# Kernel optimization log

Hardware: AMD Instinct MI355X
Metric: run time of the kernel (lower is better)

The kernel has to match this reference:

```python
import jax, jax.numpy as jnp
import numpy as np

BATCH = 32768
TEXT_DIM = 384
HIDDEN = 256
NUM_LAYERS = 4
NUM_VERTS = 12
K_NN = 6


def _build_template():
    """Icosphere vertices (12, normalized) and row-normalized kNN adjacency (12,12)."""
    phi = (1.0 + 5.0 ** 0.5) / 2.0
    v = np.array([
        [-1, phi, 0], [1, phi, 0], [-1, -phi, 0], [1, -phi, 0],
        [0, -1, phi], [0, 1, phi], [0, -1, -phi], [0, 1, -phi],
        [phi, 0, -1], [phi, 0, 1], [-phi, 0, -1], [-phi, 0, 1],
    ], dtype=np.float32)
    v = v / np.linalg.norm(v, axis=1, keepdims=True)
    dist = np.linalg.norm(v[:, None, :] - v[None, :, :], axis=-1)  # (12,12)
    # k+1 smallest per row; index 0 is self (distance 0), skip it
    idx = np.argsort(dist, axis=1, kind='stable')[:, 1:K_NN + 1]
    adj = np.zeros((NUM_VERTS, NUM_VERTS), dtype=np.float32)
    rows = np.repeat(np.arange(NUM_VERTS), K_NN)
    adj[rows, idx.reshape(-1)] = 1.0
    adj = adj / (adj.sum(axis=1, keepdims=True) + 1e-6)
    return jnp.asarray(v), jnp.asarray(adj)


def setup_inputs() -> dict:
    key = jax.random.key(0)
    ks = jax.random.split(key, 8)
    template, adjacency = _build_template()
    scale = 0.02
    return {
        "text_emb": jax.random.normal(ks[0], (BATCH, TEXT_DIM), dtype=jnp.float32),
        "W_text": jax.random.normal(ks[1], (TEXT_DIM, HIDDEN), dtype=jnp.float32) * scale,
        "b_text": jnp.zeros((HIDDEN,), dtype=jnp.float32),
        "W_gnn": jax.random.normal(ks[2], (NUM_LAYERS, HIDDEN, HIDDEN), dtype=jnp.float32) * scale,
        "b_gnn": jnp.zeros((NUM_LAYERS, HIDDEN), dtype=jnp.float32),
        "W_out": jax.random.normal(ks[3], (HIDDEN, 3), dtype=jnp.float32) * scale,
        "b_out": jnp.zeros((3,), dtype=jnp.float32),
        "adjacency": adjacency,   # (12,12) buffer
        "template": template,     # (12,3) buffer
    }


def reference(text_emb, W_text, b_text, W_gnn, b_gnn, W_out, b_out, adjacency, template):
    # text projection -> broadcast to all nodes
    tf = text_emb @ W_text + b_text                       # (B, H)
    B = text_emb.shape[0]
    h = jnp.broadcast_to(tf[:, None, :], (B, NUM_VERTS, HIDDEN))
    # GNN layers: aggregate (shared adjacency across batch), project, relu
    for l in range(NUM_LAYERS):
        agg = jnp.einsum('nm,bmd->bnd', adjacency, h)     # (B, 12, H)
        h = jax.nn.relu(agg @ W_gnn[l] + b_gnn[l])
    displacements = h @ W_out + b_out                     # (B, 12, 3)
    return template[None, :, :] + displacements
```

## Files before the change

### kernel.cpp

```cpp
#include <hip/hip_runtime.h>
#include <stdint.h>

#define TD      384
#define HID     256

typedef __bf16 bf16;
typedef __attribute__((ext_vector_type(8))) __bf16 bf16x8;
typedef __attribute__((ext_vector_type(4))) float f32x4;

union FragU { uint4 u; bf16x8 f; };
union PackU { uint4 u; bf16 v[8]; };

__device__ inline f32x4 mfma16(bf16x8 a, bf16x8 b, f32x4 c) {
  return __builtin_amdgcn_mfma_f32_16x16x32_bf16(a, b, c, 0, 0, 0);
}

__global__ __launch_bounds__(256) void prep_all(
    const float* __restrict__ W_text, const float* __restrict__ b_text,
    const float* __restrict__ W_gnn, const float* __restrict__ b_gnn,
    const float* __restrict__ W_out,
    bf16* __restrict__ wt_f, bf16* __restrict__ wt_g,
    float* __restrict__ wot, float* __restrict__ bfv)
{
  const int bid = blockIdx.x, tid = threadIdx.x;
  const float* g0 = W_gnn;
  if (bid < 48) {
    const int k0 = bid * 8;
    const int n = tid;
    float a0=0.f,a1=0.f,a2=0.f,a3=0.f,a4=0.f,a5=0.f,a6=0.f,a7=0.f;
    for (int j = 0; j < HID; j += 8) {
      #pragma unroll
      for (int u = 0; u < 8; u++) {
        float g = g0[(size_t)(j + u) * HID + n];
        a0 += W_text[(size_t)(k0 + 0) * HID + j + u] * g;
        a1 += W_text[(size_t)(k0 + 1) * HID + j + u] * g;
        a2 += W_text[(size_t)(k0 + 2) * HID + j + u] * g;
        a3 += W_text[(size_t)(k0 + 3) * HID + j + u] * g;
        a4 += W_text[(size_t)(k0 + 4) * HID + j + u] * g;
        a5 += W_text[(size_t)(k0 + 5) * HID + j + u] * g;
        a6 += W_text[(size_t)(k0 + 6) * HID + j + u] * g;
        a7 += W_text[(size_t)(k0 + 7) * HID + j + u] * g;
      }
    }
    PackU pk;
    pk.v[0]=(bf16)a0; pk.v[1]=(bf16)a1; pk.v[2]=(bf16)a2; pk.v[3]=(bf16)a3;
    pk.v[4]=(bf16)a4; pk.v[5]=(bf16)a5; pk.v[6]=(bf16)a6; pk.v[7]=(bf16)a7;
    int idx = ((n >> 4) * 48 + bid) * 16 + (n & 15);
    *(uint4*)(wt_f + idx * 8) = pk.u;
  } else if (bid < 144) {
    int idx = (bid - 48) * 256 + tid;
    int cc = idx & 15, c = idx >> 4;
    int l = c >> 9, c2 = c & 511;
    int oct = c2 & 31;
    int n = (c2 >> 5) * 16 + cc;
    const float* base = W_gnn + (size_t)(l + 1) * HID * HID;
    PackU pk;
    #pragma unroll
    for (int j = 0; j < 8; j++) pk.v[j] = (bf16)base[(oct * 8 + j) * HID + n];
    *(uint4*)(wt_g + idx * 8) = pk.u;
  } else {
    int n = tid;
    float s0 = 0.f, s1 = 0.f;
    for (int j = 0; j < HID; j += 2) {
      s0 += b_text[j]     * g0[(size_t)j * HID + n];
      s1 += b_text[j + 1] * g0[(size_t)(j + 1) * HID + n];
    }
    bfv[n] = s0 + s1 + b_gnn[n];
    #pragma unroll
    for (int t = tid; t < 3 * HID; t += 256) {
      int comp = t >> 8, k = t & 255;
      wot[comp * HID + k] = W_out[k * 3 + comp];
    }
  }
}

__global__ __launch_bounds__(256, 2) void mesh_kernel(
    const float* __restrict__ text,
    const bf16* __restrict__ wt_f,
    const bf16* __restrict__ wt_g,
    const float* __restrict__ b_f,
    const float* __restrict__ b_gnn,
    const float* __restrict__ wot,
    const float* __restrict__ b_out,
    const float* __restrict__ tmpl,
    float* __restrict__ out)
{
  __shared__ __align__(16) unsigned char smem[81920];
  unsigned char* Tbuf = smem;
  unsigned char* Hbuf = smem + 49152;
  float* dispBuf = (float*)(smem + 32768);

  const int tid  = threadIdx.x;
  const int lane = tid & 63;
  const int w    = tid >> 6;
  const int cc   = lane & 15;
  const int qq   = lane >> 4;
  const int rowbase = blockIdx.x * 64;

  f32x4 acc[4][4];

  auto zero_acc = [&]() {
    f32x4 z = {0.f, 0.f, 0.f, 0.f};
    #pragma unroll
    for (int mt = 0; mt < 4; mt++)
      #pragma unroll
      for (int nt = 0; nt < 4; nt++) acc[mt][nt] = z;
  };

  auto loadA = [&](const unsigned char* src, int rowB, int ks, bf16x8* A) {
    #pragma unroll
    for (int mt = 0; mt < 4; mt++) {
      int m = mt * 16 + cc;
      FragU fu;
      fu.u = *(const uint4*)(src + m * rowB + (((ks * 4 + qq) ^ (m & 7)) * 16));
      A[mt] = fu.f;
    }
  };

  auto loadB = [&](const char* wb, int K8, int ks, bf16x8* B) {
    #pragma unroll
    for (int nt = 0; nt < 4; nt++) {
      FragU fu;
      fu.u = *(const uint4*)(wb + (size_t)(nt * K8 + ks * 4) * 256);
      B[nt] = fu.f;
    }
  };

  auto epilogue = [&](unsigned char* dst, const float* bias_ptr, bool relu) {
    float bias4[4];
    #pragma unroll
    for (int nt = 0; nt < 4; nt++) bias4[nt] = bias_ptr[w * 64 + nt * 16 + cc];
    #pragma unroll
    for (int mt = 0; mt < 4; mt++) {
      #pragma unroll
      for (int nt = 0; nt < 4; nt++) {
        int col = w * 64 + nt * 16 + cc;
        #pragma unroll
        for (int r = 0; r < 4; r++) {
          int m = mt * 16 + qq * 4 + r;
          float v = acc[mt][nt][r] + bias4[nt];
          if (relu) v = fmaxf(v, 0.f);
          *(bf16*)(dst + m * 512 + ((col >> 3) ^ (m & 7)) * 16 + (col & 7) * 2) = (bf16)v;
        }
      }
    }
  };

  auto runLayer = [&](const unsigned char* src, const char* wb,
                      unsigned char* dst, const float* bias_ptr) {
    zero_acc();
    bf16x8 A[4], B[4], An[4], Bn[4];
    loadB(wb, 32, 0, B);
    loadA(src, 512, 0, A);
    #pragma unroll
    for (int ks = 0; ks < 8; ks++) {
      if (ks < 7) {
        loadB(wb, 32, ks + 1, Bn);
        loadA(src, 512, ks + 1, An);
      }
      #pragma unroll
      for (int mt = 0; mt < 4; mt++)
        #pragma unroll
        for (int nt = 0; nt < 4; nt++)
          acc[mt][nt] = mfma16(A[mt], B[nt], acc[mt][nt]);
      if (ks < 7) {
        #pragma unroll
        for (int t = 0; t < 4; t++) { A[t] = An[t]; B[t] = Bn[t]; }
      }
    }
    epilogue(dst, bias_ptr, true);
  };

  const float* tbase = text + (size_t)rowbase * TD;
  auto stageHalf = [&](int half) {
    #pragma unroll
    for (int i = 0; i < 6; i++) {
      int id = i * 256 + tid;
      int m = id / 24, ol = id - m * 24;
      int o = half * 24 + ol;
      const float4* p = (const float4*)(tbase + m * TD + o * 8);
      float4 x = p[0], y = p[1];
      PackU pk;
      pk.v[0]=(bf16)x.x; pk.v[1]=(bf16)x.y; pk.v[2]=(bf16)x.z; pk.v[3]=(bf16)x.w;
      pk.v[4]=(bf16)y.x; pk.v[5]=(bf16)y.y; pk.v[6]=(bf16)y.z; pk.v[7]=(bf16)y.w;
      *(uint4*)(Tbuf + m * 768 + ((o ^ (m & 7)) * 16)) = pk.u;
    }
  };

  stageHalf(0);
  __syncthreads();
  stageHalf(1);

  zero_acc();
  const char* wbf = (const char*)wt_f + (size_t)(w * 4 * 48 + qq) * 256 + cc * 16;
  {
    bf16x8 A[4], B[4], An[4], Bn[4];
    loadB(wbf, 48, 0, B);
    loadA(Tbuf, 768, 0, A);
    #pragma unroll
    for (int ks = 0; ks < 6; ks++) {
      if (ks < 5) { loadB(wbf, 48, ks + 1, Bn); loadA(Tbuf, 768, ks + 1, An); }
      #pragma unroll
      for (int mt = 0; mt < 4; mt++)
        #pragma unroll
        for (int nt = 0; nt < 4; nt++)
          acc[mt][nt] = mfma16(A[mt], B[nt], acc[mt][nt]);
      if (ks < 5) {
        #pragma unroll
        for (int t = 0; t < 4; t++) { A[t] = An[t]; B[t] = Bn[t]; }
      }
    }
    __syncthreads();
    loadB(wbf, 48, 6, B);
    loadA(Tbuf, 768, 6, A);
    #pragma unroll
    for (int ks = 6; ks < 12; ks++) {
      if (ks < 11) { loadB(wbf, 48, ks + 1, Bn); loadA(Tbuf, 768, ks + 1, An); }
      #pragma unroll
      for (int mt = 0; mt < 4; mt++)
        #pragma unroll
        for (int nt = 0; nt < 4; nt++)
          acc[mt][nt] = mfma16(A[mt], B[nt], acc[mt][nt]);
      if (ks < 11) {
        #pragma unroll
        for (int t = 0; t < 4; t++) { A[t] = An[t]; B[t] = Bn[t]; }
      }
    }
  }
  epilogue(Hbuf, b_f, true);
  __syncthreads();

  {
    const char* wg = (const char*)wt_g + (size_t)(w * 4 * 32 + qq) * 256 + cc * 16;
    runLayer(Hbuf, wg,                          Tbuf, b_gnn + 1 * HID);
    __syncthreads();
    runLayer(Tbuf, wg + (size_t)1 * HID * HID * 2, Hbuf, b_gnn + 2 * HID);
    __syncthreads();
    runLayer(Hbuf, wg + (size_t)2 * HID * HID * 2, Tbuf, b_gnn + 3 * HID);
    __syncthreads();
  }

  if (tid < 192) {
    int comp = tid >> 6;
    int r = tid & 63;
    const float4* wrow = (const float4*)(wot + comp * HID);
    float s = 0.f;
    #pragma unroll 4
    for (int o = 0; o < 32; o++) {
      FragU fu; fu.u = *(const uint4*)(Tbuf + r * 512 + ((o ^ (r & 7)) * 16));
      float4 w0 = wrow[2 * o], w1 = wrow[2 * o + 1];
      s += (float)fu.f[0]*w0.x + (float)fu.f[1]*w0.y + (float)fu.f[2]*w0.z + (float)fu.f[3]*w0.w;
      s += (float)fu.f[4]*w1.x + (float)fu.f[5]*w1.y + (float)fu.f[6]*w1.z + (float)fu.f[7]*w1.w;
    }
    dispBuf[r * 3 + comp] = s + b_out[comp];
  }
  __syncthreads();

  #pragma unroll
  for (int ii = 0; ii < 9; ii++) {
    int i = ii * 256 + tid;
    int row = i / 36;
    int j = i - row * 36;
    out[(size_t)rowbase * 36 + i] = tmpl[j] + dispBuf[row * 3 + j % 3];
  }
}

extern "C" void kernel_launch(void* const* d_in, const int* in_sizes, int n_in,
                              void* d_out, int out_size, void* d_ws, size_t ws_size,
                              hipStream_t stream) {
  const float* text   = (const float*)d_in[0];
  const float* W_text = (const float*)d_in[1];
  const float* b_text = (const float*)d_in[2];
  const float* W_gnn  = (const float*)d_in[3];
  const float* b_gnn  = (const float*)d_in[4];
  const float* W_out  = (const float*)d_in[5];
  const float* b_out  = (const float*)d_in[6];
  const float* tmpl   = (const float*)d_in[8];
  float* outp = (float*)d_out;

  float* bfv  = (float*)d_ws;
  float* wot  = bfv + HID;
  bf16* wt_f  = (bf16*)(wot + 3 * HID);
  bf16* wt_g  = wt_f + TD * HID;

  prep_all<<<145, 256, 0, stream>>>(W_text, b_text, W_gnn, b_gnn, W_out,
                                    wt_f, wt_g, wot, bfv);
  mesh_kernel<<<32768 / 64, 256, 0, stream>>>(text, wt_f, wt_g, bfv, b_gnn,
                                              wot, b_out, tmpl, outp);
}
```

Before: 138.7 us.

## Reuse single LDS buffer in place to fit three blocks per CU

```diff
diff --git a/kernel.cpp b/kernel.cpp
--- a/kernel.cpp
+++ b/kernel.cpp
@@ -74,7 +74,7 @@
   }
 }
 
-__global__ __launch_bounds__(256, 2) void mesh_kernel(
+__global__ __launch_bounds__(256, 3) void mesh_kernel(
     const float* __restrict__ text,
     const bf16* __restrict__ wt_f,
     const bf16* __restrict__ wt_g,
@@ -85,9 +85,8 @@
     const float* __restrict__ tmpl,
     float* __restrict__ out)
 {
-  __shared__ __align__(16) unsigned char smem[81920];
+  __shared__ __align__(16) unsigned char smem[49152];
   unsigned char* Tbuf = smem;
-  unsigned char* Hbuf = smem + 49152;
   float* dispBuf = (float*)(smem + 32768);
 
   const int tid  = threadIdx.x;
@@ -107,12 +106,12 @@
       for (int nt = 0; nt < 4; nt++) acc[mt][nt] = z;
   };
 
-  auto loadA = [&](const unsigned char* src, int rowB, int ks, bf16x8* A) {
+  auto loadA = [&](int rowB, int ks, bf16x8* A) {
     #pragma unroll
     for (int mt = 0; mt < 4; mt++) {
       int m = mt * 16 + cc;
       FragU fu;
-      fu.u = *(const uint4*)(src + m * rowB + (((ks * 4 + qq) ^ (m & 7)) * 16));
+      fu.u = *(const uint4*)(Tbuf + m * rowB + (((ks * 4 + qq) ^ (m & 7)) * 16));
       A[mt] = fu.f;
     }
   };
@@ -126,7 +125,7 @@
     }
   };
 
-  auto epilogue = [&](unsigned char* dst, const float* bias_ptr, bool relu) {
+  auto epilogue = [&](const float* bias_ptr) {
     float bias4[4];
     #pragma unroll
     for (int nt = 0; nt < 4; nt++) bias4[nt] = bias_ptr[w * 64 + nt * 16 + cc];
@@ -138,26 +137,21 @@
         #pragma unroll
         for (int r = 0; r < 4; r++) {
           int m = mt * 16 + qq * 4 + r;
-          float v = acc[mt][nt][r] + bias4[nt];
-          if (relu) v = fmaxf(v, 0.f);
-          *(bf16*)(dst + m * 512 + ((col >> 3) ^ (m & 7)) * 16 + (col & 7) * 2) = (bf16)v;
+          float v = fmaxf(acc[mt][nt][r] + bias4[nt], 0.f);
+          *(bf16*)(Tbuf + m * 512 + ((col >> 3) ^ (m & 7)) * 16 + (col & 7) * 2) = (bf16)v;
         }
       }
     }
   };
 
-  auto runLayer = [&](const unsigned char* src, const char* wb,
-                      unsigned char* dst, const float* bias_ptr) {
+  auto runLayer = [&](const char* wb, const float* bias_ptr) {
     zero_acc();
-    bf16x8 A[4], B[4], An[4], Bn[4];
+    bf16x8 A[4], B[4], Bn[4];
     loadB(wb, 32, 0, B);
-    loadA(src, 512, 0, A);
     #pragma unroll
     for (int ks = 0; ks < 8; ks++) {
-      if (ks < 7) {
-        loadB(wb, 32, ks + 1, Bn);
-        loadA(src, 512, ks + 1, An);
-      }
+      if (ks < 7) loadB(wb, 32, ks + 1, Bn);
+      loadA(512, ks, A);
       #pragma unroll
       for (int mt = 0; mt < 4; mt++)
         #pragma unroll
@@ -165,10 +159,12 @@
           acc[mt][nt] = mfma16(A[mt], B[nt], acc[mt][nt]);
       if (ks < 7) {
         #pragma unroll
-        for (int t = 0; t < 4; t++) { A[t] = An[t]; B[t] = Bn[t]; }
-      }
-    }
-    epilogue(dst, bias_ptr, true);
+        for (int t = 0; t < 4; t++) B[t] = Bn[t];
+      }
+    }
+    __syncthreads();
+    epilogue(bias_ptr);
+    __syncthreads();
   };
 
   const float* tbase = text + (size_t)rowbase * TD;
@@ -194,28 +190,25 @@
   zero_acc();
   const char* wbf = (const char*)wt_f + (size_t)(w * 4 * 48 + qq) * 256 + cc * 16;
   {
-    bf16x8 A[4], B[4], An[4], Bn[4];
+    bf16x8 A[4], B[4], Bn[4];
     loadB(wbf, 48, 0, B);
-    loadA(Tbuf, 768, 0, A);
     #pragma unroll
     for (int ks = 0; ks < 6; ks++) {
-      if (ks < 5) { loadB(wbf, 48, ks + 1, Bn); loadA(Tbuf, 768, ks + 1, An); }
+      loadB(wbf, 48, ks + 1, Bn);
+      loadA(768, ks, A);
       #pragma unroll
       for (int mt = 0; mt < 4; mt++)
         #pragma unroll
         for (int nt = 0; nt < 4; nt++)
           acc[mt][nt] = mfma16(A[mt], B[nt], acc[mt][nt]);
-      if (ks < 5) {
-        #pragma unroll
-        for (int t = 0; t < 4; t++) { A[t] = An[t]; B[t] = Bn[t]; }
-      }
+      #pragma unroll
+      for (int t = 0; t < 4; t++) B[t] = Bn[t];
     }
     __syncthreads();
-    loadB(wbf, 48, 6, B);
-    loadA(Tbuf, 768, 6, A);
     #pragma unroll
     for (int ks = 6; ks < 12; ks++) {
-      if (ks < 11) { loadB(wbf, 48, ks + 1, Bn); loadA(Tbuf, 768, ks + 1, An); }
+      if (ks < 11) loadB(wbf, 48, ks + 1, Bn);
+      loadA(768, ks, A);
       #pragma unroll
       for (int mt = 0; mt < 4; mt++)
         #pragma unroll
@@ -223,21 +216,19 @@
           acc[mt][nt] = mfma16(A[mt], B[nt], acc[mt][nt]);
       if (ks < 11) {
         #pragma unroll
-        for (int t = 0; t < 4; t++) { A[t] = An[t]; B[t] = Bn[t]; }
-      }
-    }
-  }
-  epilogue(Hbuf, b_f, true);
+        for (int t = 0; t < 4; t++) B[t] = Bn[t];
+      }
+    }
+  }
+  __syncthreads();
+  epilogue(b_f);
   __syncthreads();
 
   {
     const char* wg = (const char*)wt_g + (size_t)(w * 4 * 32 + qq) * 256 + cc * 16;
-    runLayer(Hbuf, wg,                          Tbuf, b_gnn + 1 * HID);
-    __syncthreads();
-    runLayer(Tbuf, wg + (size_t)1 * HID * HID * 2, Hbuf, b_gnn + 2 * HID);
-    __syncthreads();
-    runLayer(Hbuf, wg + (size_t)2 * HID * HID * 2, Tbuf, b_gnn + 3 * HID);
-    __syncthreads();
+    runLayer(wg,                             b_gnn + 1 * HID);
+    runLayer(wg + (size_t)1 * HID * HID * 2, b_gnn + 2 * HID);
+    runLayer(wg + (size_t)2 * HID * HID * 2, b_gnn + 3 * HID);
   }
 
   if (tid < 192) {
```

Measured after the change: 151.4 us. 9.2% more time.
